# Kernel optimization log

Measured on AMD Instinct MI355X. Metric: run time of the kernel, lower is better.

Reference implementation:

```python
import jax, jax.numpy as jnp
import numpy as np

N_UNI = 32; N_G = 4; N_PPG = 8
MAX_D = 100.0; MIN_D = 0.5
SOM_SIGMA = 2.0; G_STD = 2.5
ORIG = jnp.array([-25.6, -25.6, -2.0], jnp.float32); VS = 0.4
NZ = 16; GW = 128; GL = 128; DIM = 128
H_IMG = 352; W_IMG = 1216

def pe(x):
    # positional encoding: num_freqs=6, include_input -> 3 + 36 = 39 dims
    f = 2.0 ** jnp.arange(6, dtype=x.dtype)
    xf = x[..., None] * f  # (...,3,6)
    s = x.shape[:-1]
    return jnp.concatenate([x, jnp.sin(xf).reshape(s + (18,)), jnp.cos(xf).reshape(s + (18,))], axis=-1)

def resnet_fc(z, x, P):
    # pixelNeRF-style ResnetFC with latent injection per block
    w_in, b_in, wz, bz, w0, b0, w1, b1, w_out, b_out = P
    h = x @ w_in + b_in
    for i in range(3):
        h = h + z @ wz[i] + bz[i]
        net = jax.nn.relu(h) @ w0[i] + b0[i]
        h = h + jax.nn.relu(net) @ w1[i] + b1[i]
    return jax.nn.relu(h) @ w_out + b_out

def trilinear(grid, pts):
    # grid: (NZ,GW,GL,DIM); pts: (N,3) lidar coords -> trilinear gather, 0 outside
    g = (pts - ORIG) / VS
    gx, gy, gz = g[:, 0], g[:, 1], g[:, 2]
    inb = (gx >= 0) & (gx <= GW - 1) & (gy >= 0) & (gy <= GL - 1) & (gz >= 0) & (gz <= NZ - 1)
    gx = jnp.clip(gx, 0.0, GW - 1.0); gy = jnp.clip(gy, 0.0, GL - 1.0); gz = jnp.clip(gz, 0.0, NZ - 1.0)
    x0 = jnp.clip(jnp.floor(gx).astype(jnp.int32), 0, GW - 2)
    y0 = jnp.clip(jnp.floor(gy).astype(jnp.int32), 0, GL - 2)
    z0 = jnp.clip(jnp.floor(gz).astype(jnp.int32), 0, NZ - 2)
    fx = gx - x0; fy = gy - y0; fz = gz - z0
    def c(zi, xi, yi, w):
        return grid[zi, xi, yi] * w[:, None]
    feat = (c(z0, x0, y0, (1 - fz) * (1 - fx) * (1 - fy)) + c(z0, x0, y0 + 1, (1 - fz) * (1 - fx) * fy)
            + c(z0, x0 + 1, y0, (1 - fz) * fx * (1 - fy)) + c(z0, x0 + 1, y0 + 1, (1 - fz) * fx * fy)
            + c(z0 + 1, x0, y0, fz * (1 - fx) * (1 - fy)) + c(z0 + 1, x0, y0 + 1, fz * (1 - fx) * fy)
            + c(z0 + 1, x0 + 1, y0, fz * fx * (1 - fy)) + c(z0 + 1, x0 + 1, y0 + 1, fz * fx * fy))
    return feat * inb[:, None].astype(feat.dtype)

def bilinear(img, uv):
    # img: (3,H,W); uv: (N,2) (u=col, v=row) -> (N,3)
    _, H, W = img.shape
    u = jnp.clip(uv[:, 0], 0.0, W - 1.0); v = jnp.clip(uv[:, 1], 0.0, H - 1.0)
    u0 = jnp.clip(jnp.floor(u).astype(jnp.int32), 0, W - 2)
    v0 = jnp.clip(jnp.floor(v).astype(jnp.int32), 0, H - 2)
    fu = u - u0; fv = v - v0
    g = lambda vi, ui: img[:, vi, ui]
    out = (g(v0, u0) * ((1 - fv) * (1 - fu)) + g(v0, u0 + 1) * ((1 - fv) * fu)
           + g(v0 + 1, u0) * (fv * (1 - fu)) + g(v0 + 1, u0 + 1) * (fv * fu))
    return out.T

def _forward(bev_feature, cam_K, img_source, img_target, T_source2infer, T_source2target,
             gaussian_noise, Pm, Pg, sampled_pixels):
    R = sampled_pixels.shape[0]
    # (B, C, W, L) -> (n_z, W, L, dim)
    vf = bev_feature[0].reshape(NZ, DIM, GW, GL).transpose(0, 2, 3, 1)
    inv_K = jnp.linalg.inv(cam_K)
    pix = sampled_pixels.astype(jnp.float32)
    homog = jnp.concatenate([pix, jnp.ones((R, 1), jnp.float32)], axis=1)
    dirs = homog @ inv_K.T
    unit = dirs / jnp.linalg.norm(dirs, axis=1, keepdims=True)  # (R,3) cam frame
    Rsi = T_source2infer[:3, :3]; tsi = T_source2infer[:3, 3]
    viewdir = unit @ Rsi.T  # lidar frame

    # --- predict per-ray gaussian means/stds at coarse segment centers ---
    base = (jnp.arange(N_G, dtype=jnp.float32) + 0.5) * (MAX_D / N_G)
    pg = (unit[:, None, :] * base[None, :, None]).reshape(-1, 3) @ Rsi.T + tsi
    fg = trilinear(vf, pg)
    vdg = jnp.broadcast_to(viewdir[:, None, :], (R, N_G, 3)).reshape(-1, 3)
    og = resnet_fc(fg, jnp.concatenate([pe(pg), vdg], axis=1), Pg)  # (R*N_G,2)
    means = jnp.clip(base[None, :] + og[:, 0].reshape(R, N_G), MIN_D, MAX_D)
    stds = G_STD * jax.nn.sigmoid(og[:, 1].reshape(R, N_G)) + 0.1

    # --- sample points: uniform + gaussian, sorted along ray ---
    d_g = jnp.clip(means[:, :, None] + stds[:, :, None] * gaussian_noise, MIN_D, MAX_D).reshape(R, N_G * N_PPG)
    d_u = jnp.broadcast_to(jnp.linspace(MIN_D, MAX_D, N_UNI, dtype=jnp.float32)[None, :], (R, N_UNI))
    d = jnp.sort(jnp.concatenate([d_u, d_g], axis=1), axis=1)  # (R,64)
    P = d.shape[1]
    pl = (unit[:, None, :] * d[..., None]).reshape(-1, 3) @ Rsi.T + tsi
    fl = trilinear(vf, pl)
    vd = jnp.broadcast_to(viewdir[:, None, :], (R, P, 3)).reshape(-1, 3)
    out = resnet_fc(fl, jnp.concatenate([pe(pl), vd], axis=1), Pm).reshape(R, P, 4)
    sigma = jax.nn.softplus(out[..., 0]); rgb = jax.nn.sigmoid(out[..., 1:])

    # --- volume rendering ---
    deltas = jnp.concatenate([d[:, 1:] - d[:, :-1], jnp.full((R, 1), 1e10, jnp.float32)], axis=1)
    alpha = 1.0 - jnp.exp(-sigma * deltas)
    trans = jnp.cumprod(1.0 - alpha + 1e-10, axis=1)
    trans = jnp.concatenate([jnp.ones((R, 1), jnp.float32), trans[:, :-1]], axis=1)
    w = alpha * trans
    depth = (w * d).sum(axis=1)          # (R,)
    color = (w[..., None] * rgb).sum(axis=1)  # (R,3)

    # --- losses ---
    diff = jnp.abs(means - jax.lax.stop_gradient(depth)[:, None])
    loss_dist = diff.min(axis=1)
    pdf = jnp.exp(-(d[:, None, :] - means[..., None]) ** 2 / (2.0 * stds[..., None] ** 2)) / (stds[..., None] * jnp.sqrt(2.0 * jnp.pi))
    loss_kl = (w * (-jnp.log(pdf.mean(axis=1) + 1e-6))).sum(axis=1)
    src = bilinear(img_source, pix)
    loss_color = jnp.abs(src - color)
    pcam = unit * depth[:, None]
    pt = pcam @ T_source2target[:3, :3].T + T_source2target[:3, 3]
    proj = pt @ cam_K.T
    uv = proj[:, :2] / jnp.clip(proj[:, 2:3], 1e-3)
    tgt = bilinear(img_target, uv)
    loss_reproj = jnp.abs(src - tgt)
    total = loss_reproj.mean() + loss_color.mean() + loss_kl.mean() + 0.01 * loss_dist.mean()
    return total

def setup_inputs() -> dict:
    key = jax.random.key(0)
    def rn(i, shape, s=1.0):
        return jax.random.normal(jax.random.fold_in(key, i), shape, jnp.float32) * s
    R = 4096
    inp = {}
    inp['bev_feature'] = rn(0, (1, NZ * DIM, GW, GL), 0.5)
    inp['cam_K'] = jnp.array([[720.0, 0.0, 608.0], [0.0, 720.0, 176.0], [0.0, 0.0, 1.0]], jnp.float32)
    inp['img_source'] = jax.random.uniform(jax.random.fold_in(key, 1), (3, H_IMG, W_IMG), jnp.float32)
    inp['img_target'] = jax.random.uniform(jax.random.fold_in(key, 2), (3, H_IMG, W_IMG), jnp.float32)
    Rcl = jnp.array([[0.0, 0.0, 1.0], [-1.0, 0.0, 0.0], [0.0, -1.0, 0.0]], jnp.float32)  # cam->lidar axes
    inp['T_source2infer'] = jnp.eye(4, dtype=jnp.float32).at[:3, :3].set(Rcl).at[:3, 3].set(jnp.array([0.5, 0.2, 0.1], jnp.float32))
    inp['T_source2target'] = jnp.eye(4, dtype=jnp.float32).at[0, 3].set(0.8).at[1, 3].set(0.05)
    inp['gaussian_noise'] = rn(3, (R, N_G, N_PPG))
    u = jax.random.randint(jax.random.fold_in(key, 4), (R,), 0, W_IMG)
    v = jax.random.randint(jax.random.fold_in(key, 5), (R,), 0, H_IMG)
    inp['sampled_pixels'] = jnp.stack([u, v], axis=1).astype(jnp.int32)
    for pfx, (i0, d_out) in {'m': (10, 4), 'g': (40, 2)}.items():
        inp[pfx + '_w_in'] = rn(i0, (42, 128), 0.05)
        inp[pfx + '_b_in'] = jnp.zeros((128,), jnp.float32)
        inp[pfx + '_wz'] = rn(i0 + 1, (3, 128, 128), 0.05)
        inp[pfx + '_bz'] = jnp.zeros((3, 128), jnp.float32)
        inp[pfx + '_w0'] = rn(i0 + 2, (3, 128, 128), 0.05)
        inp[pfx + '_b0'] = jnp.zeros((3, 128), jnp.float32)
        inp[pfx + '_w1'] = rn(i0 + 3, (3, 128, 128), 0.05)
        inp[pfx + '_b1'] = jnp.zeros((3, 128), jnp.float32)
        inp[pfx + '_w_out'] = rn(i0 + 4, (128, d_out), 0.05)
        inp[pfx + '_b_out'] = jnp.zeros((d_out,), jnp.float32)
    return inp

def reference(bev_feature, cam_K, img_source, img_target, T_source2infer, T_source2target,
              gaussian_noise, sampled_pixels,
              m_w_in, m_b_in, m_wz, m_bz, m_w0, m_b0, m_w1, m_b1, m_w_out, m_b_out,
              g_w_in, g_b_in, g_wz, g_bz, g_w0, g_b0, g_w1, g_b1, g_w_out, g_b_out):
    Pm = (m_w_in, m_b_in, m_wz, m_bz, m_w0, m_b0, m_w1, m_b1, m_w_out, m_b_out)
    Pg = (g_w_in, g_b_in, g_wz, g_bz, g_w0, g_b0, g_w1, g_b1, g_w_out, g_b_out)
    return _forward(bev_feature, cam_K, img_source, img_target, T_source2infer, T_source2target,
                    gaussian_noise, Pm, Pg, sampled_pixels)
```

## Files before the change

### kernel.cpp

```cpp
#include <hip/hip_runtime.h>

typedef __attribute__((ext_vector_type(8))) short short8;
typedef __attribute__((ext_vector_type(4))) float f32x4;
typedef __attribute__((ext_vector_type(2))) float f32x2;
typedef __attribute__((ext_vector_type(2))) unsigned u32x2;
typedef unsigned short ushort_t;

#define WIMG 1216
#define HIMG 352

__device__ __forceinline__ float sigmoid_(float x){ return 1.f/(1.f+__expf(-x)); }
__device__ __forceinline__ float softplus_(float x){
  return fmaxf(x,0.f) + log1pf(__expf(-fabsf(x)));
}
__device__ __forceinline__ ushort_t f2b(float x){
  union { float f; unsigned u; } v; v.f = x;
  unsigned r = v.u + 0x7FFF + ((v.u >> 16) & 1);
  return (ushort_t)(r >> 16);
}
__device__ __forceinline__ ushort_t f2b_fast(float x){
  union { float f; unsigned u; } v; v.f = x;
  return (ushort_t)((v.u + 0x8000u) >> 16);
}
__device__ __forceinline__ unsigned pack_trunc(float a, float b){
  union { float f; unsigned u; } va, vb; va.f = a; vb.f = b;
  return (va.u >> 16) | (vb.u & 0xFFFF0000u);
}
__device__ __forceinline__ f32x2 bf2x(unsigned u){
  union { unsigned uu[2]; f32x2 f; } v;
  v.uu[0] = u << 16; v.uu[1] = u & 0xFFFF0000u;
  return v.f;
}

__global__ __launch_bounds__(256)
void k_prep(const float* __restrict__ bev, ushort_t* __restrict__ vfh, int mode,
            const float* __restrict__ mw_in, const float* __restrict__ mwz,
            const float* __restrict__ mw0, const float* __restrict__ mw1,
            const float* __restrict__ mwo,
            const float* __restrict__ gw_in, const float* __restrict__ gwz,
            const float* __restrict__ gw0, const float* __restrict__ gw1,
            const float* __restrict__ gwo,
            ushort_t* __restrict__ pkM, ushort_t* __restrict__ pkG,
            float* __restrict__ out0){
  int bx = blockIdx.x;
  int tid = threadIdx.x;
  if (bx < 8192) {
    if (!mode) return;
    __shared__ float tile[64][65];
    int y0 = (bx & 1) * 64;
    int c0 = ((bx >> 1) & 1) * 64;
    int zx = bx >> 2;
    const float* s = bev + (size_t)(zx >> 7)*2097152 + (size_t)c0*16384 + (size_t)(zx & 127)*128 + y0;
    int r0 = tid >> 4, f4 = tid & 15;
    #pragma unroll
    for (int it = 0; it < 4; ++it) {
      int c = it*16 + r0;
      f32x4 v = __builtin_nontemporal_load((const f32x4*)(s + (size_t)c*16384 + f4*4));
      tile[c][f4*4+0]=v.x; tile[c][f4*4+1]=v.y; tile[c][f4*4+2]=v.z; tile[c][f4*4+3]=v.w;
    }
    __syncthreads();
    ushort_t* d = vfh + ((size_t)zx*128 + y0)*128 + c0;
    #pragma unroll
    for (int it = 0; it < 4; ++it) {
      int y = it*16 + r0;
      u32x2 o;
      o.x = pack_trunc(tile[f4*4+0][y], tile[f4*4+1][y]);
      o.y = pack_trunc(tile[f4*4+2][y], tile[f4*4+3][y]);
      __builtin_nontemporal_store(o, (u32x2*)(d + (size_t)y*128 + f4*4));
    }
    return;
  }
  int pb = bx - 8192;
  if (pb == 0 && tid == 0) out0[0] = 0.f;
  int net = pb >= 624;
  const float* w_in = net ? gw_in : mw_in;
  const float* wz   = net ? gwz   : mwz;
  const float* w0   = net ? gw0   : mw0;
  const float* w1   = net ? gw1   : mw1;
  const float* wo   = net ? gwo   : mwo;
  int outd = net ? 2 : 4;
  ushort_t* pk = net ? pkG : pkM;
  int id = (pb - (net ? 624 : 0))*256 + tid;
  if (id >= 39*4096) return;
  int blk = id >> 12;
  int e = id & 4095;
  float val = 0.f;
  if (blk < 38) {
    int nt = e >> 9, lane = (e >> 3) & 63, j = e & 7;
    int kloc = (lane >> 4)*8 + j;
    int n = nt*16 + (lane & 15);
    if (blk < 2) {
      int k = blk*32 + kloc;
      val = (k < 42) ? w_in[k*128 + n] : 0.f;
    } else {
      int g = blk - 2;
      int i = g / 12, r = g % 12, m = r >> 2, ks = r & 3;
      int k = ks*32 + kloc;
      const float* src = (m==0 ? wz : (m==1 ? w0 : w1)) + i*16384;
      val = src[k*128 + n];
    }
  } else if (e < 2048) {
    int ks = e >> 9, lane = (e >> 3) & 63, j = e & 7;
    int k = ks*32 + (lane >> 4)*8 + j;
    int n = lane & 15;
    val = (n < outd) ? wo[k*outd + n] : 0.f;
  }
  pk[id] = f2b(val);
}

template<int KS>
__device__ __forceinline__ void gemm_frag(const ushort_t* lds,
                                          const ushort_t* __restrict__ pkW,
                                          f32x4 acc[2][4], int wave, int lane)
{
  short8 w[KS][2];
  #pragma unroll
  for (int ks = 0; ks < KS; ++ks)
    #pragma unroll
    for (int ct = 0; ct < 2; ++ct)
      w[ks][ct] = *(const short8*)(pkW + (size_t)((ks*8 + wave*2 + ct)*64 + lane)*8);
  #pragma unroll
  for (int ks = 0; ks < KS; ++ks) {
    short8 b[4];
    #pragma unroll
    for (int nt = 0; nt < 4; ++nt)
      b[nt] = *(const short8*)(lds + (ks*4 + nt)*512 + lane*8);
    #pragma unroll
    for (int ct = 0; ct < 2; ++ct)
      #pragma unroll
      for (int nt = 0; nt < 4; ++nt)
        acc[ct][nt] = __builtin_amdgcn_mfma_f32_16x16x32_bf16(w[ks][ct], b[nt], acc[ct][nt], 0,0,0);
  }
}

__device__ __forceinline__ void store_reluF(ushort_t* buf, const f32x4 acc[2][4],
                                            int wave, int lane){
  int l15 = lane & 15, quad = lane >> 4;
  int j = (quad & 1)*4;
  #pragma unroll
  for (int ct = 0; ct < 2; ++ct) {
    int lp = (ct*2 + (quad >> 1))*16 + l15;
    #pragma unroll
    for (int nt = 0; nt < 4; ++nt) {
      uint2 o;
      o.x = pack_trunc(fmaxf(acc[ct][nt][0],0.f), fmaxf(acc[ct][nt][1],0.f));
      o.y = pack_trunc(fmaxf(acc[ct][nt][2],0.f), fmaxf(acc[ct][nt][3],0.f));
      *(uint2*)(buf + (wave*4 + nt)*512 + lp*8 + j) = o;
    }
  }
}

template<int OUTD>
__global__ __launch_bounds__(256, 4)
void k_fused(const ushort_t* __restrict__ vfh, const float* __restrict__ vf0, int mode,
             const float* __restrict__ camK, const int* __restrict__ pix,
             const float* __restrict__ noise,
             float* __restrict__ unit, float* __restrict__ viewdir,
             const float* __restrict__ Tsi, float* __restrict__ dsort,
             const ushort_t* __restrict__ pk,
             const float* __restrict__ b_in, const float* __restrict__ bzv,
             const float* __restrict__ b0v, const float* __restrict__ b1v,
             const float* __restrict__ b_out,
             float* __restrict__ means, float* __restrict__ stds, float* __restrict__ outbuf)
{
  __shared__ int   sOff[64];
  __shared__ float sW[64][8];
  __shared__ float sPx[64], sPy[64], sPz[64];
  __shared__ float sUx[16], sUy[16], sUz[16], sVx[16], sVy[16], sVz[16];
  __shared__ float sMean[64], sStd[64];
  __shared__ __align__(16) ushort_t zf[16*512];
  __shared__ __align__(16) ushort_t Wb[16*512];

  int tid = threadIdx.x;
  int qbase = blockIdx.x * 64;

  if constexpr (OUTD == 2) {
    if (tid < 16) {
      int gray = (qbase >> 2) + tid;
      float a=camK[0],b=camK[1],c=camK[2],d=camK[3],e=camK[4],f=camK[5],g=camK[6],h=camK[7],i=camK[8];
      float c00 = e*i-f*h, c01 = c*h-b*i, c02 = b*f-c*e;
      float c10 = f*g-d*i, c11 = a*i-c*g, c12 = c*d-a*f;
      float c20 = d*h-e*g, c21 = b*g-a*h, c22 = a*e-b*d;
      float det = a*c00 + b*c10 + c*c20;
      float id = 1.f/det;
      float u = (float)pix[2*gray], v = (float)pix[2*gray+1];
      float dx = (c00*u + c01*v + c02)*id;
      float dy = (c10*u + c11*v + c12)*id;
      float dz = (c20*u + c21*v + c22)*id;
      float n = sqrtf(dx*dx+dy*dy+dz*dz);
      dx/=n; dy/=n; dz/=n;
      sUx[tid]=dx; sUy[tid]=dy; sUz[tid]=dz;
      unit[3*gray]=dx; unit[3*gray+1]=dy; unit[3*gray+2]=dz;
      float vx = Tsi[0]*dx + Tsi[1]*dy + Tsi[2]*dz;
      float vy = Tsi[4]*dx + Tsi[5]*dy + Tsi[6]*dz;
      float vz = Tsi[8]*dx + Tsi[9]*dy + Tsi[10]*dz;
      sVx[tid]=vx; sVy[tid]=vy; sVz[tid]=vz;
      viewdir[3*gray]=vx; viewdir[3*gray+1]=vy; viewdir[3*gray+2]=vz;
    }
  } else {
    if (tid == 0) {
      int ray = blockIdx.x;
      sUx[0]=unit[3*ray]; sUy[0]=unit[3*ray+1]; sUz[0]=unit[3*ray+2];
      sVx[0]=viewdir[3*ray]; sVy[0]=viewdir[3*ray+1]; sVz[0]=viewdir[3*ray+2];
    }
  }
  __syncthreads();

  if (tid < 64) {
    float t, ux, uy, uz;
    if constexpr (OUTD == 2) {
      t = ((float)(tid & 3) + 0.5f) * 25.f;
      int lr = tid >> 2;
      ux = sUx[lr]; uy = sUy[lr]; uz = sUz[lr];
    } else {
      t = dsort[qbase + tid];
      ux = sUx[0]; uy = sUy[0]; uz = sUz[0];
    }
    float wx=ux*t, wy=uy*t, wz=uz*t;
    float px = Tsi[0]*wx + Tsi[1]*wy + Tsi[2]*wz + Tsi[3];
    float py = Tsi[4]*wx + Tsi[5]*wy + Tsi[6]*wz + Tsi[7];
    float pz = Tsi[8]*wx + Tsi[9]*wy + Tsi[10]*wz + Tsi[11];
    sPx[tid]=px; sPy[tid]=py; sPz[tid]=pz;
    float gx = (px + 25.6f)*2.5f;
    float gy = (py + 25.6f)*2.5f;
    float gz = (pz + 2.0f)*2.5f;
    bool inb = (gx>=0.f)&&(gx<=127.f)&&(gy>=0.f)&&(gy<=127.f)&&(gz>=0.f)&&(gz<=15.f);
    gx = fminf(fmaxf(gx,0.f),127.f);
    gy = fminf(fmaxf(gy,0.f),127.f);
    gz = fminf(fmaxf(gz,0.f),15.f);
    int x0 = min(max((int)floorf(gx),0),126);
    int y0 = min(max((int)floorf(gy),0),126);
    int z0 = min(max((int)floorf(gz),0),14);
    float fx = gx-(float)x0, fy = gy-(float)y0, fz = gz-(float)z0;
    float sc = inb ? 1.f : 0.f;
    float ax0 = 1.f-fx, ay0 = 1.f-fy;
    float az0 = (1.f-fz)*sc, az1 = fz*sc;
    float q00 = ax0*ay0, q01 = ax0*fy, q10 = fx*ay0, q11 = fx*fy;
    sW[tid][0] = az0*q00; sW[tid][1] = az0*q01; sW[tid][2] = az0*q10; sW[tid][3] = az0*q11;
    sW[tid][4] = az1*q00; sW[tid][5] = az1*q01; sW[tid][6] = az1*q10; sW[tid][7] = az1*q11;
    sOff[tid] = mode ? (((z0*128 + x0)*128 + y0)*128)
                     : (z0*2097152 + x0*128 + y0);
  }
  __syncthreads();

  for (int it = 0; it < 4; ++it) {
    int lin = it*256 + tid;
    int p = lin >> 4, cb = lin & 15;
    float4 wA = *(const float4*)&sW[p][0];
    float4 wB = *(const float4*)&sW[p][4];
    f32x2 r01={0.f,0.f}, r23={0.f,0.f}, r45={0.f,0.f}, r67={0.f,0.f};
    if (mode) {
      const ushort_t* b = vfh + sOff[p] + cb*8;
      uint4 v;
      #define ACC8(PTR, W) \
        v = *(const uint4*)(PTR); \
        r01 += (W)*bf2x(v.x); r23 += (W)*bf2x(v.y); \
        r45 += (W)*bf2x(v.z); r67 += (W)*bf2x(v.w);
      ACC8(b,                     wA.x)
      ACC8(b + 128,               wA.y)
      ACC8(b + 16384,             wA.z)
      ACC8(b + 16384 + 128,       wA.w)
      ACC8(b + 2097152,           wB.x)
      ACC8(b + 2097152 + 128,     wB.y)
      ACC8(b + 2097152 + 16384,   wB.z)
      ACC8(b + 2097152 + 16512,   wB.w)
      #undef ACC8
    } else {
      const float* bsrc = vf0 + sOff[p];
      float rr[8];
      #pragma unroll
      for (int k = 0; k < 8; ++k) {
        const float* bc = bsrc + (size_t)(cb*8 + k)*16384;
        rr[k] = wA.x*bc[0] + wA.y*bc[1] + wA.z*bc[128] + wA.w*bc[129]
              + wB.x*bc[2097152] + wB.y*bc[2097153] + wB.z*bc[2097280] + wB.w*bc[2097281];
      }
      r01 = (f32x2){rr[0],rr[1]}; r23 = (f32x2){rr[2],rr[3]};
      r45 = (f32x2){rr[4],rr[5]}; r67 = (f32x2){rr[6],rr[7]};
    }
    uint4 o;
    o.x = pack_trunc(r01.x, r01.y); o.y = pack_trunc(r23.x, r23.y);
    o.z = pack_trunc(r45.x, r45.y); o.w = pack_trunc(r67.x, r67.y);
    int T = (cb >> 2)*4 + (p >> 4);
    int lanep = (cb & 3)*16 + (p & 15);
    *(uint4*)(zf + T*512 + lanep*8) = o;
  }

  {
    int p = tid & 63, dg = tid >> 6;
    float px = sPx[p], py = sPy[p], pz = sPz[p];
    int lr = (OUTD == 2) ? (p >> 2) : 0;
    float vx = sVx[lr], vy = sVy[lr], vz = sVz[lr];
    #pragma unroll 1
    for (int it = 0; it < 16; ++it) {
      int d = it*4 + dg;
      float val = 0.f;
      if (d < 3)      val = (d==0)?px:((d==1)?py:pz);
      else if (d < 39) {
        int s = d - 3; bool isSin = (s < 18); if (!isSin) s -= 18;
        int axis = s/6, fi = s%6;
        float base = (axis==0)?px:((axis==1)?py:pz);
        float arg = base * (float)(1 << fi);
        val = isSin ? __sinf(arg) : __cosf(arg);
      } else if (d < 42) {
        val = (d==39)?vx:((d==40)?vy:vz);
      }
      int addr = (d>>5)*2048 + (p>>4)*512 + (((d>>3)&3)*16 + (p&15))*8 + (d&7);
      Wb[addr] = f2b_fast(val);
    }
  }
  __syncthreads();

  int wave = tid >> 6, lane = tid & 63;
  int l15 = lane & 15, quad = lane >> 4;
  int cbase = wave*32 + quad*4;

  f32x4 h[2][4];
  #pragma unroll
  for (int ct = 0; ct < 2; ++ct) {
    f32x4 bi = *(const f32x4*)(b_in + cbase + ct*16);
    #pragma unroll
    for (int nt = 0; nt < 4; ++nt) h[ct][nt] = bi;
  }
  gemm_frag<2>(Wb, pk, h, wave, lane);

  const ushort_t* pkl = pk + 2*4096;
  #pragma unroll 1
  for (int i3 = 0; i3 < 3; ++i3) {
    gemm_frag<4>(zf, pkl + (size_t)(i3*12)*4096, h, wave, lane);
    #pragma unroll
    for (int ct = 0; ct < 2; ++ct) {
      f32x4 bz = *(const f32x4*)(bzv + i3*128 + cbase + ct*16);
      #pragma unroll
      for (int nt = 0; nt < 4; ++nt) h[ct][nt] += bz;
    }
    __syncthreads();
    store_reluF(Wb, h, wave, lane);
    __syncthreads();
    f32x4 net[2][4];
    #pragma unroll
    for (int ct = 0; ct < 2; ++ct) {
      f32x4 c0b = *(const f32x4*)(b0v + i3*128 + cbase + ct*16);
      #pragma unroll
      for (int nt = 0; nt < 4; ++nt) net[ct][nt] = c0b;
    }
    gemm_frag<4>(Wb, pkl + (size_t)(i3*12+4)*4096, net, wave, lane);
    __syncthreads();
    store_reluF(Wb, net, wave, lane);
    __syncthreads();
    gemm_frag<4>(Wb, pkl + (size_t)(i3*12+8)*4096, h, wave, lane);
    #pragma unroll
    for (int ct = 0; ct < 2; ++ct) {
      f32x4 o1b = *(const f32x4*)(b1v + i3*128 + cbase + ct*16);
      #pragma unroll
      for (int nt = 0; nt < 4; ++nt) h[ct][nt] += o1b;
    }
  }
  __syncthreads();
  store_reluF(Wb, h, wave, lane);
  __syncthreads();

  {
    const ushort_t* pkw = pk + 38*4096;
    f32x4 oa = (f32x4){0.f,0.f,0.f,0.f};
    #pragma unroll
    for (int ks = 0; ks < 4; ++ks) {
      short8 w = *(const short8*)(pkw + (size_t)(ks*64 + lane)*8);
      short8 b = *(const short8*)(Wb + (ks*4 + wave)*512 + lane*8);
      oa = __builtin_amdgcn_mfma_f32_16x16x32_bf16(w, b, oa, 0,0,0);
    }
    if (quad == 0) {
      int lq = wave*16 + l15;
      int q = qbase + lq;
      if constexpr (OUTD == 4) {
        float4 o = { oa[0] + b_out[0], oa[1] + b_out[1], oa[2] + b_out[2], oa[3] + b_out[3] };
        *(float4*)(outbuf + (size_t)q*4) = o;
      } else {
        int g = q & 3;
        float m = fminf(fmaxf(((float)g + 0.5f)*25.f + oa[0] + b_out[0], 0.5f), 100.f);
        float sd = 2.5f*sigmoid_(oa[1] + b_out[1]) + 0.1f;
        means[q] = m; stds[q] = sd;
        sMean[lq] = m; sStd[lq] = sd;
      }
    }
  }

  if constexpr (OUTD == 2) {
    __syncthreads();
    float* fbuf = (float*)zf;
    int lr = tid >> 4;
    int sbase = (tid & 15) * 4;
    float vals[4];
    #pragma unroll
    for (int t = 0; t < 4; ++t) {
      int slot = sbase + t;
      float val;
      if (slot < 32) val = 0.5f + (float)slot * (99.5f/31.f);
      else {
        int idx = slot - 32, g = idx >> 3, s = idx & 7;
        int lq = lr*4 + g;
        float mu = sMean[lq], sd = sStd[lq];
        val = fminf(fmaxf(mu + sd*noise[(size_t)(qbase + lq)*8 + s], 0.5f), 100.f);
      }
      fbuf[lr*64 + slot] = val;
      vals[t] = val;
    }
    __syncthreads();
    int rk[4] = {0,0,0,0};
    for (int k = 0; k < 64; ++k) {
      float o = fbuf[lr*64 + k];
      #pragma unroll
      for (int t = 0; t < 4; ++t)
        rk[t] += (o < vals[t]) || (o == vals[t] && k < sbase + t);
    }
    int gray = (qbase >> 2) + lr;
    #pragma unroll
    for (int t = 0; t < 4; ++t)
      dsort[(size_t)gray*64 + rk[t]] = vals[t];
  }
}

__device__ __forceinline__ void bilin3(const float* __restrict__ img, float u, float v, float* out){
  u = fminf(fmaxf(u, 0.f), (float)(WIMG-1));
  v = fminf(fmaxf(v, 0.f), (float)(HIMG-1));
  int u0 = min(max((int)floorf(u),0), WIMG-2);
  int v0 = min(max((int)floorf(v),0), HIMG-2);
  float fu = u - (float)u0, fv = v - (float)v0;
  float w00=(1.f-fv)*(1.f-fu), w01=(1.f-fv)*fu, w10=fv*(1.f-fu), w11=fv*fu;
  #pragma unroll
  for (int c = 0; c < 3; ++c) {
    const float* b = img + (size_t)c*(HIMG*WIMG) + (size_t)v0*WIMG + u0;
    out[c] = w00*b[0] + w01*b[1] + w10*b[WIMG] + w11*b[WIMG+1];
  }
}

__global__ void k_render(const float* __restrict__ outbuf, const float* __restrict__ dsort,
                         const float* __restrict__ means, const float* __restrict__ stds,
                         const float* __restrict__ unit,
                         const float* __restrict__ img_src, const float* __restrict__ img_tgt,
                         const int* __restrict__ pix, const float* __restrict__ camK,
                         const float* __restrict__ Tst, float* __restrict__ loss_out, int R){
  __shared__ float accw[4];
  int gid = blockIdx.x*blockDim.x + threadIdx.x;
  int r = gid >> 6, lane = gid & 63;
  float d = dsort[(size_t)r*64 + lane];
  float dn = __shfl_down(d, 1);
  float delta = (lane < 63) ? (dn - d) : 1e10f;
  float4 o = *(const float4*)(outbuf + (size_t)r*256 + lane*4);
  float sig = softplus_(o.x);
  float alpha = 1.f - __expf(-sig*delta);
  float om = 1.f - alpha + 1e-10f;
  float prod = om;
  #pragma unroll
  for (int off = 1; off < 64; off <<= 1) {
    float v = __shfl_up(prod, off);
    if (lane >= off) prod *= v;
  }
  float texc = __shfl_up(prod, 1);
  if (lane == 0) texc = 1.f;
  float w = alpha * texc;
  float m0=means[r*4],m1=means[r*4+1],m2=means[r*4+2],m3=means[r*4+3];
  float s0=stds[r*4], s1=stds[r*4+1], s2=stds[r*4+2], s3=stds[r*4+3];
  float t0=(d-m0)/s0, t1=(d-m1)/s1, t2=(d-m2)/s2, t3=(d-m3)/s3;
  float pm = 0.25f*0.3989422804014327f*(__expf(-0.5f*t0*t0)/s0 + __expf(-0.5f*t1*t1)/s1
                                      + __expf(-0.5f*t2*t2)/s2 + __expf(-0.5f*t3*t3)/s3);
  float kl  = w * (-__logf(pm + 1e-6f));
  float dep = w * d;
  float c0 = w * sigmoid_(o.y);
  float c1 = w * sigmoid_(o.z);
  float c2 = w * sigmoid_(o.w);
  #pragma unroll
  for (int off = 32; off; off >>= 1) {
    dep += __shfl_xor(dep, off);
    c0  += __shfl_xor(c0, off);
    c1  += __shfl_xor(c1, off);
    c2  += __shfl_xor(c2, off);
    kl  += __shfl_xor(kl, off);
  }
  if (lane == 0) {
    float ld = fminf(fminf(fabsf(m0-dep),fabsf(m1-dep)), fminf(fabsf(m2-dep),fabsf(m3-dep)));
    float src[3], tgt[3];
    float u = (float)pix[2*r], v = (float)pix[2*r+1];
    bilin3(img_src, u, v, src);
    float ux=unit[3*r],uy=unit[3*r+1],uz=unit[3*r+2];
    float pcx=ux*dep, pcy=uy*dep, pcz=uz*dep;
    float ptx = Tst[0]*pcx + Tst[1]*pcy + Tst[2]*pcz + Tst[3];
    float pty = Tst[4]*pcx + Tst[5]*pcy + Tst[6]*pcz + Tst[7];
    float ptz = Tst[8]*pcx + Tst[9]*pcy + Tst[10]*pcz + Tst[11];
    float prx = camK[0]*ptx + camK[1]*pty + camK[2]*ptz;
    float pry = camK[3]*ptx + camK[4]*pty + camK[5]*ptz;
    float prz = camK[6]*ptx + camK[7]*pty + camK[8]*ptz;
    prz = fmaxf(prz, 0.001f);
    bilin3(img_tgt, prx/prz, pry/prz, tgt);
    float lrepr = fabsf(src[0]-tgt[0])+fabsf(src[1]-tgt[1])+fabsf(src[2]-tgt[2]);
    float lcol  = fabsf(src[0]-c0)+fabsf(src[1]-c1)+fabsf(src[2]-c2);
    float invR = 1.f/(float)R;
    accw[threadIdx.x >> 6] = (lrepr + lcol) * (invR/3.f) + kl*invR + 0.01f*ld*invR;
  }
  __syncthreads();
  if (threadIdx.x == 0)
    atomicAdd(loss_out, accw[0]+accw[1]+accw[2]+accw[3]);
}

extern "C" void kernel_launch(void* const* d_in, const int* in_sizes, int n_in,
                              void* d_out, int out_size, void* d_ws, size_t ws_size,
                              hipStream_t stream)
{
  const float* bev   = (const float*)d_in[0];
  const float* camK  = (const float*)d_in[1];
  const float* img_s = (const float*)d_in[2];
  const float* img_t = (const float*)d_in[3];
  const float* Tsi   = (const float*)d_in[4];
  const float* Tst   = (const float*)d_in[5];
  const float* noise = (const float*)d_in[6];
  const int*   pix   = (const int*)d_in[7];
  const float* m_w_in=(const float*)d_in[8];  const float* m_b_in=(const float*)d_in[9];
  const float* m_wz  =(const float*)d_in[10]; const float* m_bz  =(const float*)d_in[11];
  const float* m_w0  =(const float*)d_in[12]; const float* m_b0  =(const float*)d_in[13];
  const float* m_w1  =(const float*)d_in[14]; const float* m_b1  =(const float*)d_in[15];
  const float* m_wo  =(const float*)d_in[16]; const float* m_bo  =(const float*)d_in[17];
  const float* g_w_in=(const float*)d_in[18]; const float* g_b_in=(const float*)d_in[19];
  const float* g_wz  =(const float*)d_in[20]; const float* g_bz  =(const float*)d_in[21];
  const float* g_w0  =(const float*)d_in[22]; const float* g_b0  =(const float*)d_in[23];
  const float* g_w1  =(const float*)d_in[24]; const float* g_b1  =(const float*)d_in[25];
  const float* g_wo  =(const float*)d_in[26]; const float* g_bo  =(const float*)d_in[27];

  int R = in_sizes[7] / 2;
  float* ws = (float*)d_ws;
  size_t off = 0;
  float* unitb = ws + off; off += (size_t)R*3;
  float* vdirb = ws + off; off += (size_t)R*3;
  float* means = ws + off; off += (size_t)R*4;
  float* stds  = ws + off; off += (size_t)R*4;
  float* dsort = ws + off; off += (size_t)R*64;
  float* outbf = ws + off; off += (size_t)R*256;
  ushort_t* pkM = (ushort_t*)(ws + off);
  ushort_t* pkG = pkM + 39*4096;
  off += 39*4096 + 64;
  off = (off + 63) & ~(size_t)63;
  ushort_t* vfh = (ushort_t*)(ws + off);
  size_t need = off*4ull + (size_t)16*128*128*128*2ull;
  int mode = (ws_size >= need) ? 1 : 0;

  k_prep<<<9440,256,0,stream>>>(bev, vfh, mode,
      m_w_in,m_wz,m_w0,m_w1,m_wo, g_w_in,g_wz,g_w0,g_w1,g_wo,
      pkM, pkG, (float*)d_out);
  k_fused<2><<<R/16,256,0,stream>>>(vfh,bev,mode,camK,pix,noise,unitb,vdirb,Tsi,dsort,pkG,
      g_b_in,g_bz,g_b0,g_b1,g_bo, means,stds,nullptr);
  k_fused<4><<<R,256,0,stream>>>(vfh,bev,mode,camK,pix,noise,unitb,vdirb,Tsi,dsort,pkM,
      m_b_in,m_bz,m_b0,m_b1,m_bo, means,stds,outbf);
  k_render<<<R/4,256,0,stream>>>(outbf,dsort,means,stds,unitb,img_s,img_t,pix,camK,Tst,
                                 (float*)d_out,R);
}
```

Baseline: 438.9 us.

## Swizzle latent LDS tile, vectorize PE staging, use hardware bf16 pack and MFMA priority

The latent-feature tile in LDS now uses an XOR swizzle, applied on both the write side and the read side in gemm_frag, to cut bank conflicts on the 16-byte reads. The positional-encoding staging now computes eight values per thread and writes them as one packed 16-byte store instead of sixteen scalar bf16 stores. Truncating bf16 packing is replaced with the v_cvt_pk_bf16_f32 instruction, which changes rounding from truncation to round-to-nearest. s_setprio is raised around the MFMA blocks to favour matrix issue across waves.

Measured after the change: 429.7 us. -2.1%, faster.

```diff
diff --git a/kernel.cpp b/kernel.cpp
--- a/kernel.cpp
+++ b/kernel.cpp
@@ -18,13 +18,14 @@
   unsigned r = v.u + 0x7FFF + ((v.u >> 16) & 1);
   return (ushort_t)(r >> 16);
 }
-__device__ __forceinline__ ushort_t f2b_fast(float x){
-  union { float f; unsigned u; } v; v.f = x;
-  return (ushort_t)((v.u + 0x8000u) >> 16);
-}
 __device__ __forceinline__ unsigned pack_trunc(float a, float b){
   union { float f; unsigned u; } va, vb; va.f = a; vb.f = b;
   return (va.u >> 16) | (vb.u & 0xFFFF0000u);
+}
+__device__ __forceinline__ unsigned cvt_pk_bf16(float a, float b){
+  unsigned r;
+  asm("v_cvt_pk_bf16_f32 %0, %1, %2" : "=v"(r) : "v"(a), "v"(b));
+  return r;
 }
 __device__ __forceinline__ f32x2 bf2x(unsigned u){
   union { unsigned uu[2]; f32x2 f; } v;
@@ -108,7 +109,7 @@
   pk[id] = f2b(val);
 }
 
-template<int KS>
+template<int KS, bool SWZ>
 __device__ __forceinline__ void gemm_frag(const ushort_t* lds,
                                           const ushort_t* __restrict__ pkW,
                                           f32x4 acc[2][4], int wave, int lane)
@@ -121,15 +122,18 @@
       w[ks][ct] = *(const short8*)(pkW + (size_t)((ks*8 + wave*2 + ct)*64 + lane)*8);
   #pragma unroll
   for (int ks = 0; ks < KS; ++ks) {
+    int idx = SWZ ? ((lane & ~7) | ((lane ^ (lane >> 3) ^ ks) & 7)) : lane;
     short8 b[4];
     #pragma unroll
     for (int nt = 0; nt < 4; ++nt)
-      b[nt] = *(const short8*)(lds + (ks*4 + nt)*512 + lane*8);
+      b[nt] = *(const short8*)(lds + (ks*4 + nt)*512 + idx*8);
+    __builtin_amdgcn_s_setprio(1);
     #pragma unroll
     for (int ct = 0; ct < 2; ++ct)
       #pragma unroll
       for (int nt = 0; nt < 4; ++nt)
         acc[ct][nt] = __builtin_amdgcn_mfma_f32_16x16x32_bf16(w[ks][ct], b[nt], acc[ct][nt], 0,0,0);
+    __builtin_amdgcn_s_setprio(0);
   }
 }
 
@@ -143,8 +147,8 @@
     #pragma unroll
     for (int nt = 0; nt < 4; ++nt) {
       uint2 o;
-      o.x = pack_trunc(fmaxf(acc[ct][nt][0],0.f), fmaxf(acc[ct][nt][1],0.f));
-      o.y = pack_trunc(fmaxf(acc[ct][nt][2],0.f), fmaxf(acc[ct][nt][3],0.f));
+      o.x = cvt_pk_bf16(fmaxf(acc[ct][nt][0],0.f), fmaxf(acc[ct][nt][1],0.f));
+      o.y = cvt_pk_bf16(fmaxf(acc[ct][nt][2],0.f), fmaxf(acc[ct][nt][3],0.f));
       *(uint2*)(buf + (wave*4 + nt)*512 + lp*8 + j) = o;
     }
   }
@@ -278,34 +282,45 @@
       r45 = (f32x2){rr[4],rr[5]}; r67 = (f32x2){rr[6],rr[7]};
     }
     uint4 o;
-    o.x = pack_trunc(r01.x, r01.y); o.y = pack_trunc(r23.x, r23.y);
-    o.z = pack_trunc(r45.x, r45.y); o.w = pack_trunc(r67.x, r67.y);
+    o.x = cvt_pk_bf16(r01.x, r01.y); o.y = cvt_pk_bf16(r23.x, r23.y);
+    o.z = cvt_pk_bf16(r45.x, r45.y); o.w = cvt_pk_bf16(r67.x, r67.y);
     int T = (cb >> 2)*4 + (p >> 4);
     int lanep = (cb & 3)*16 + (p & 15);
-    *(uint4*)(zf + T*512 + lanep*8) = o;
+    int lsw = (lanep & ~7) | ((lanep ^ (lanep >> 3) ^ (cb >> 2)) & 7);
+    *(uint4*)(zf + T*512 + lsw*8) = o;
   }
 
   {
-    int p = tid & 63, dg = tid >> 6;
+    int p = tid & 63, wv = tid >> 6;
     float px = sPx[p], py = sPy[p], pz = sPz[p];
     int lr = (OUTD == 2) ? (p >> 2) : 0;
     float vx = sVx[lr], vy = sVy[lr], vz = sVz[lr];
-    #pragma unroll 1
-    for (int it = 0; it < 16; ++it) {
-      int d = it*4 + dg;
-      float val = 0.f;
-      if (d < 3)      val = (d==0)?px:((d==1)?py:pz);
-      else if (d < 39) {
-        int s = d - 3; bool isSin = (s < 18); if (!isSin) s -= 18;
-        int axis = s/6, fi = s%6;
-        float base = (axis==0)?px:((axis==1)?py:pz);
-        float arg = base * (float)(1 << fi);
-        val = isSin ? __sinf(arg) : __cosf(arg);
-      } else if (d < 42) {
-        val = (d==39)?vx:((d==40)?vy:vz);
+    #pragma unroll
+    for (int hf = 0; hf < 2; ++hf) {
+      int g = hf*4 + wv;
+      float vals[8];
+      #pragma unroll
+      for (int j = 0; j < 8; ++j) {
+        int d = g*8 + j;
+        float val = 0.f;
+        if (d < 3)      val = (d==0)?px:((d==1)?py:pz);
+        else if (d < 39) {
+          int s = d - 3; bool isSin = (s < 18); if (!isSin) s -= 18;
+          int axis = s/6, fi = s%6;
+          float base = (axis==0)?px:((axis==1)?py:pz);
+          float arg = base * (float)(1 << fi);
+          val = isSin ? __sinf(arg) : __cosf(arg);
+        } else if (d < 42) {
+          val = (d==39)?vx:((d==40)?vy:vz);
+        }
+        vals[j] = val;
       }
-      int addr = (d>>5)*2048 + (p>>4)*512 + (((d>>3)&3)*16 + (p&15))*8 + (d&7);
-      Wb[addr] = f2b_fast(val);
+      uint4 o;
+      o.x = cvt_pk_bf16(vals[0], vals[1]);
+      o.y = cvt_pk_bf16(vals[2], vals[3]);
+      o.z = cvt_pk_bf16(vals[4], vals[5]);
+      o.w = cvt_pk_bf16(vals[6], vals[7]);
+      *(uint4*)(Wb + (g>>2)*2048 + (p>>4)*512 + ((g&3)*16 + (p&15))*8) = o;
     }
   }
   __syncthreads();
@@ -321,12 +336,12 @@
     #pragma unroll
     for (int nt = 0; nt < 4; ++nt) h[ct][nt] = bi;
   }
-  gemm_frag<2>(Wb, pk, h, wave, lane);
+  gemm_frag<2,false>(Wb, pk, h, wave, lane);
 
   const ushort_t* pkl = pk + 2*4096;
   #pragma unroll 1
   for (int i3 = 0; i3 < 3; ++i3) {
-    gemm_frag<4>(zf, pkl + (size_t)(i3*12)*4096, h, wave, lane);
+    gemm_frag<4,true>(zf, pkl + (size_t)(i3*12)*4096, h, wave, lane);
     #pragma unroll
     for (int ct = 0; ct < 2; ++ct) {
       f32x4 bz = *(const f32x4*)(bzv + i3*128 + cbase + ct*16);
@@ -343,11 +358,11 @@
       #pragma unroll
       for (int nt = 0; nt < 4; ++nt) net[ct][nt] = c0b;
     }
-    gemm_frag<4>(Wb, pkl + (size_t)(i3*12+4)*4096, net, wave, lane);
+    gemm_frag<4,false>(Wb, pkl + (size_t)(i3*12+4)*4096, net, wave, lane);
     __syncthreads();
     store_reluF(Wb, net, wave, lane);
     __syncthreads();
-    gemm_frag<4>(Wb, pkl + (size_t)(i3*12+8)*4096, h, wave, lane);
+    gemm_frag<4,false>(Wb, pkl + (size_t)(i3*12+8)*4096, h, wave, lane);
     #pragma unroll
     for (int ct = 0; ct < 2; ++ct) {
       f32x4 o1b = *(const f32x4*)(b1v + i3*128 + cbase + ct*16);
```
